# Kernel optimization log

Measured on AMD Instinct MI355X. Metric: run time of the kernel, lower is better.

The kernel has to match this reference:

```python
import jax, jax.numpy as jnp
import numpy as np

NUM_HEADS = 12
HIDDEN = 768
HEAD = HIDDEN // NUM_HEADS
SCALE = HIDDEN ** (-0.5)  # NB: module scales by hidden_dim**-0.5, not head_size**-0.5


def setup_inputs() -> dict:
    key = jax.random.key(0)
    ks = jax.random.split(key, 8)
    B, N = 16, 512
    std = HIDDEN ** (-0.5)
    return {
        "x": jax.random.normal(ks[0], (B, N, HIDDEN), dtype=jnp.float32),
        "encoding_bias": jax.random.normal(ks[1], (B, N, N), dtype=jnp.float32),
        "Wq": jax.random.normal(ks[2], (HIDDEN, HIDDEN), dtype=jnp.float32) * std,
        "Wk": jax.random.normal(ks[3], (HIDDEN, HIDDEN), dtype=jnp.float32) * std,
        "Wv": jax.random.normal(ks[4], (HIDDEN, HIDDEN), dtype=jnp.float32) * std,
        "bv": jax.random.normal(ks[5], (HIDDEN,), dtype=jnp.float32) * 0.01,
        "Wo": jax.random.normal(ks[6], (HIDDEN, HIDDEN), dtype=jnp.float32) * std,
        "bo": jax.random.normal(ks[7], (HIDDEN,), dtype=jnp.float32) * 0.01,
    }


def reference(x, encoding_bias, Wq, Wk, Wv, bv, Wo, bo):
    B, N, _ = x.shape
    # torch nn.Linear: y = x @ W.T (+ b)
    q = (x @ Wq.T).reshape(B, N, NUM_HEADS, HEAD)
    k = (x @ Wk.T).reshape(B, N, NUM_HEADS, HEAD)
    v = (x @ Wv.T + bv).reshape(B, N, NUM_HEADS, HEAD)
    # scores: [B, H, N, N] with additive graph bias broadcast over heads
    a = jnp.einsum("bnhd,bmhd->bhnm", q, k) * SCALE + encoding_bias[:, None, :, :]
    # data-dependent pad mask: rows whose scores are identically zero
    pad_mask = jnp.all(a == 0, axis=-1)  # [B, H, N]
    a = jnp.where(pad_mask[..., None], -jnp.inf, a)
    a = jax.nn.softmax(a, axis=-1)
    a = jnp.nan_to_num(a)  # all -inf rows -> NaN -> 0
    o = jnp.einsum("bhnm,bmhd->bnhd", a, v).reshape(B, N, HIDDEN)
    # dropout is identity in eval mode
    return o @ Wo.T + bo
```

## Files before the change

### kernel.cpp

```cpp
#include <hip/hip_runtime.h>
#include <stdint.h>

typedef unsigned short u16;
typedef unsigned int u32;
typedef __bf16 bf16x8 __attribute__((ext_vector_type(8)));
typedef float f32x4 __attribute__((ext_vector_type(4)));

#define NH 12
#define HD 64
#define SEQ 512
#define BATCH 16
#define HID 768
#define SCALE_Q 0.03608439182435161f

__device__ __forceinline__ u16 f2bf(float f) {
    u32 u = __builtin_bit_cast(u32, f);
    u32 r = (u + 0x7FFFu + ((u >> 16) & 1u)) >> 16;
    return (u16)r;
}
__device__ __forceinline__ float bf2f(u16 h) {
    return __builtin_bit_cast(float, (u32)h << 16);
}

__device__ __forceinline__ void gl2lds16(const u16* g, u16* lds_base) {
    __builtin_amdgcn_global_load_lds(
        (const __attribute__((address_space(1))) u32*)g,
        (__attribute__((address_space(3))) u32*)lds_base, 16, 0, 0);
}

#define NXB 6144
#define NEB 4096
#define NWB 576
__global__ void cvt_all(const float* __restrict__ x, const float* __restrict__ eb,
                        const float* __restrict__ w0, const float* __restrict__ w1,
                        const float* __restrict__ w2, const float* __restrict__ w3,
                        u16* __restrict__ dst) {
    int b = blockIdx.x;
    const float* s; int sb;
    if (b < NXB) { s = x; sb = 0; }
    else if (b < NXB + NEB) { s = eb; sb = NXB; }
    else if (b < NXB + NEB + NWB) { s = w0; sb = NXB + NEB; }
    else if (b < NXB + NEB + 2 * NWB) { s = w1; sb = NXB + NEB + NWB; }
    else if (b < NXB + NEB + 3 * NWB) { s = w2; sb = NXB + NEB + 2 * NWB; }
    else { s = w3; sb = NXB + NEB + 3 * NWB; }
    int li = (b - sb) * 1024 + threadIdx.x * 4;
    float4 v = *(const float4*)(s + li);
    ushort4 o;
    o.x = f2bf(v.x); o.y = f2bf(v.y); o.z = f2bf(v.z); o.w = f2bf(v.w);
    *(ushort4*)(dst + (size_t)b * 1024 + threadIdx.x * 4) = o;
}

__device__ __forceinline__ void stage_gemm(
    const u16* __restrict__ Ag, const u16* __restrict__ Bg, int k0,
    u16* As, u16* Bs, int r0, int q0, int r1, int q1, int w)
{
    gl2lds16(Ag + (size_t)r0 * HID + k0 + q0, As + w * 512);
    gl2lds16(Ag + (size_t)r1 * HID + k0 + q1, As + 2048 + w * 512);
    gl2lds16(Bg + (size_t)r0 * HID + k0 + q0, Bs + w * 512);
    gl2lds16(Bg + (size_t)r1 * HID + k0 + q1, Bs + 2048 + w * 512);
}

__device__ __forceinline__ void gemm_mainloop(
    const u16* __restrict__ Ag, const u16* __restrict__ Bg,
    u16 (*As)[128 * 32], u16 (*Bs)[128 * 32], f32x4 (&acc)[4][4])
{
    const int tid = threadIdx.x;
    const int l = tid & 63, w = tid >> 6;
    const int wm = w & 1, wn = w >> 1;
    const int lr = l & 15, lg = l >> 4;

    const int c0 = tid, c1 = tid + 256;
    const int r0 = c0 >> 2, q0 = (((c0 & 3) ^ ((r0 >> 1) & 3)) * 8);
    const int r1 = c1 >> 2, q1 = (((c1 & 3) ^ ((r1 >> 1) & 3)) * 8);

    const int sA = (lg ^ ((lr >> 1) & 3)) * 8;

    stage_gemm(Ag, Bg, 0, As[0], Bs[0], r0, q0, r1, q1, w);
    stage_gemm(Ag, Bg, 32, As[1], Bs[1], r0, q0, r1, q1, w);

    int cur = 0;
    for (int i = 0; i < 24; i++) {
        if (i < 23)
            asm volatile("s_waitcnt vmcnt(4) lgkmcnt(0)" ::: "memory");
        else
            asm volatile("s_waitcnt vmcnt(0) lgkmcnt(0)" ::: "memory");
        __builtin_amdgcn_s_barrier();
        __builtin_amdgcn_sched_barrier(0);

        int nxt = cur + 2; if (nxt >= 3) nxt -= 3;
        if (i < 22)
            stage_gemm(Ag, Bg, (i + 2) * 32, As[nxt], Bs[nxt], r0, q0, r1, q1, w);

        bf16x8 af[4], bfr[4];
#pragma unroll
        for (int mi = 0; mi < 4; mi++)
            af[mi] = *(const bf16x8*)(As[cur] + (wm * 64 + mi * 16 + lr) * 32 + sA);
#pragma unroll
        for (int ni = 0; ni < 4; ni++)
            bfr[ni] = *(const bf16x8*)(Bs[cur] + (wn * 64 + ni * 16 + lr) * 32 + sA);
#pragma unroll
        for (int mi = 0; mi < 4; mi++)
#pragma unroll
            for (int ni = 0; ni < 4; ni++)
                acc[mi][ni] = __builtin_amdgcn_mfma_f32_16x16x32_bf16(af[mi], bfr[ni], acc[mi][ni], 0, 0, 0);

        cur += 1; if (cur >= 3) cur -= 3;
    }
}

__global__ __launch_bounds__(256, 3) void gemm_qkv(
    const u16* __restrict__ xb, const u16* __restrict__ wq,
    const u16* __restrict__ wk, const u16* __restrict__ wv,
    const float* __restrict__ bv,
    u16* __restrict__ qtb, u16* __restrict__ kb, u16* __restrict__ vtb)
{
    __shared__ __align__(16) u16 As[3][128 * 32];
    __shared__ __align__(16) u16 Bs[3][128 * 32];
    const int tid = threadIdx.x;
    const int l = tid & 63, w = tid >> 6;
    const int wm = w & 1, wn = w >> 1;
    const int lr = l & 15, lg = l >> 4;
    const int mt = blockIdx.x, nt = blockIdx.y, z = blockIdx.z;

    const u16* Bw = (z == 0) ? wq : (z == 1) ? wk : wv;
    const u16* Ag = xb + (size_t)(mt * 128) * HID;
    const u16* Bg = Bw + (size_t)(nt * 128) * HID;

    f32x4 acc[4][4] = {};
    gemm_mainloop(Ag, Bg, As, Bs, acc);

    const float sc = (z == 0) ? SCALE_Q : 1.0f;
#pragma unroll
    for (int mi = 0; mi < 4; mi++) {
#pragma unroll
        for (int ni = 0; ni < 4; ni++) {
            const int jg = nt * 128 + wn * 64 + ni * 16 + lr;
            const int h = jg >> 6, d = jg & 63;
            const int i0 = mt * 128 + wm * 64 + mi * 16 + lg * 4;
            const int b = i0 >> 9, n0 = i0 & 511;
            if (z == 1) {
#pragma unroll
                for (int r2 = 0; r2 < 4; r2++)
                    kb[((size_t)(b * NH + h) * SEQ + n0 + r2) * HD + d] = f2bf(acc[mi][ni][r2]);
            } else {
                float bb = (z == 2) ? bv[jg] : 0.0f;
                ushort4 pk;
                pk.x = f2bf(fmaf(acc[mi][ni][0], sc, bb));
                pk.y = f2bf(fmaf(acc[mi][ni][1], sc, bb));
                pk.z = f2bf(fmaf(acc[mi][ni][2], sc, bb));
                pk.w = f2bf(fmaf(acc[mi][ni][3], sc, bb));
                u16* O = (z == 0) ? qtb : vtb;
                *(ushort4*)(O + ((size_t)(b * NH + h) * HD + d) * SEQ + n0) = pk;
            }
        }
    }
}

__global__ __launch_bounds__(256, 3) void gemm_out(
    const u16* __restrict__ A, const u16* __restrict__ wo,
    const float* __restrict__ bo, float* __restrict__ Cout)
{
    __shared__ __align__(16) u16 As[3][128 * 32];
    __shared__ __align__(16) u16 Bs[3][128 * 32];
    const int tid = threadIdx.x;
    const int l = tid & 63, w = tid >> 6;
    const int wm = w & 1, wn = w >> 1;
    const int lr = l & 15, lg = l >> 4;

    const int L = blockIdx.x;
    const int xcd = L & 7, s = L >> 3;
    const int nt = s >> 3;
    const int mt = xcd * 8 + (s & 7);

    const u16* Ag = A + (size_t)(mt * 128) * HID;
    const u16* Bg = wo + (size_t)(nt * 128) * HID;

    f32x4 acc[4][4] = {};
    gemm_mainloop(Ag, Bg, As, Bs, acc);

#pragma unroll
    for (int mi = 0; mi < 4; mi++) {
#pragma unroll
        for (int ni = 0; ni < 4; ni++) {
            const int jg = nt * 128 + wn * 64 + ni * 16 + lr;
            float bb = bo[jg];
#pragma unroll
            for (int r2 = 0; r2 < 4; r2++) {
                int ig = mt * 128 + wm * 64 + mi * 16 + lg * 4 + r2;
                Cout[(size_t)ig * HID + jg] = acc[mi][ni][r2] + bb;
            }
        }
    }
}

__device__ __forceinline__ void stage_kv(
    const u16* __restrict__ Kg, const u16* __restrict__ Vg, int mt0,
    u16* Ksb, u16* Vsb, int kr0, int kc0, int kr1, int kc1, int w)
{
    gl2lds16(Kg + (size_t)(mt0 + kr0) * HD + kc0 * 8, Ksb + w * 512);
    gl2lds16(Kg + (size_t)(mt0 + kr1) * HD + kc1 * 8, Ksb + 2048 + w * 512);
    gl2lds16(Vg + (size_t)kr0 * SEQ + mt0 + kc0 * 8, Vsb + w * 512);
    gl2lds16(Vg + (size_t)kr1 * SEQ + mt0 + kc1 * 8, Vsb + 2048 + w * 512);
}

__global__ __launch_bounds__(256, 3) void attn_kernel(
    const u16* __restrict__ qtb, const u16* __restrict__ kb, const u16* __restrict__ vtb,
    const u16* __restrict__ ebb, u16* __restrict__ ob)
{
    __shared__ __align__(16) u16 Ks[2][64 * 64];
    __shared__ __align__(16) u16 Vs[2][64 * 64];
    __shared__ __align__(16) u16 Ps[8][16 * 64];

    const int tid = threadIdx.x;
    const int l = tid & 63, w = tid >> 6;
    const int lr = l & 15, lg = l >> 4;

    const int L = blockIdx.x;
    const int xcd = L & 7, s = L >> 3;
    const int b = xcd * 2 + (s / 48);
    const int s2 = s % 48;
    const int h = s2 >> 2, qt = s2 & 3;

    const int bh = b * NH + h;
    const int qrow0 = qt * 128 + w * 16;

    const u16* Kg = kb + (size_t)bh * SEQ * HD;
    const u16* Vg = vtb + (size_t)bh * HD * SEQ;
    const u16* Eg0 = ebb + ((size_t)b * SEQ + qrow0 + lg * 4) * SEQ;
    const u16* Eg1 = Eg0 + (size_t)64 * SEQ;

    const int p0 = tid, p1 = tid + 256;
    const int kr0 = p0 >> 3, kc0 = (p0 & 7) ^ (kr0 & 7);
    const int kr1 = p1 >> 3, kc1 = (p1 & 7) ^ (kr1 & 7);

    stage_kv(Kg, Vg, 0, Ks[0], Vs[0], kr0, kc0, kr1, kc1, w);

    const u16* Qg = qtb + (size_t)bh * HD * SEQ + qrow0 + lr;
    bf16x8 qA0, qA1, qB0, qB1;
#pragma unroll
    for (int j = 0; j < 8; j++) {
        qA0[j] = __builtin_bit_cast(__bf16, Qg[(size_t)(lg * 8 + j) * SEQ]);
        qA1[j] = __builtin_bit_cast(__bf16, Qg[(size_t)(lg * 8 + j + 32) * SEQ]);
        qB0[j] = __builtin_bit_cast(__bf16, Qg[(size_t)(lg * 8 + j) * SEQ + 64]);
        qB1[j] = __builtin_bit_cast(__bf16, Qg[(size_t)(lg * 8 + j + 32) * SEQ + 64]);
    }

    bf16x8 ones;
#pragma unroll
    for (int j = 0; j < 8; j++) ones[j] = __builtin_bit_cast(__bf16, (u16)0x3F80);

    f32x4 oacc0[4] = {}, oacc1[4] = {};
    f32x4 lacc0 = {}, lacc1 = {};
    float amax0[4] = {0.f, 0.f, 0.f, 0.f};
    float amax1[4] = {0.f, 0.f, 0.f, 0.f};
    u16* Pw0 = Ps[w];
    u16* Pw1 = Ps[4 + w];

    for (int t = 0; t < 8; t++) {
        const int cur = t & 1;
        const int mt0 = t * 64;
        __syncthreads();

        u16 bl0[4][4], bl1[4][4];
#pragma unroll
        for (int mi = 0; mi < 4; mi++)
#pragma unroll
            for (int r = 0; r < 4; r++) {
                bl0[mi][r] = Eg0[(size_t)r * SEQ + mt0 + mi * 16 + lr];
                bl1[mi][r] = Eg1[(size_t)r * SEQ + mt0 + mi * 16 + lr];
            }

        if (t < 7)
            stage_kv(Kg, Vg, mt0 + 64, Ks[cur ^ 1], Vs[cur ^ 1], kr0, kc0, kr1, kc1, w);

        float sm0[4][4], sm1[4][4];
#pragma unroll
        for (int mi = 0; mi < 4; mi++) {
            const int row = mi * 16 + lr;
            bf16x8 kf0 = *(const bf16x8*)(Ks[cur] + row * 64 + ((lg ^ (row & 7)) * 8));
            bf16x8 kf1 = *(const bf16x8*)(Ks[cur] + row * 64 + (((4 + lg) ^ (row & 7)) * 8));
            f32x4 s0, s1;
#pragma unroll
            for (int r = 0; r < 4; r++) { s0[r] = bf2f(bl0[mi][r]); s1[r] = bf2f(bl1[mi][r]); }
            s0 = __builtin_amdgcn_mfma_f32_16x16x32_bf16(qA0, kf0, s0, 0, 0, 0);
            s0 = __builtin_amdgcn_mfma_f32_16x16x32_bf16(qA1, kf1, s0, 0, 0, 0);
            s1 = __builtin_amdgcn_mfma_f32_16x16x32_bf16(qB0, kf0, s1, 0, 0, 0);
            s1 = __builtin_amdgcn_mfma_f32_16x16x32_bf16(qB1, kf1, s1, 0, 0, 0);
#pragma unroll
            for (int r = 0; r < 4; r++) {
                float a = s0[r], c = s1[r];
                amax0[r] = fmaxf(amax0[r], fabsf(a));
                amax1[r] = fmaxf(amax1[r], fabsf(c));
                sm0[mi][r] = __expf(a);
                sm1[mi][r] = __expf(c);
            }
        }

#pragma unroll
        for (int mi = 0; mi < 4; mi++)
#pragma unroll
            for (int r = 0; r < 4; r++) {
                const int q = lg * 4 + r;
                const int chunk = mi * 2 + (lr >> 3);
                const int off = q * 64 + ((chunk ^ (q & 7)) * 8) + (lr & 7);
                Pw0[off] = f2bf(sm0[mi][r]);
                Pw1[off] = f2bf(sm1[mi][r]);
            }

#pragma unroll
        for (int ks = 0; ks < 2; ks++) {
            bf16x8 pf0 = *(const bf16x8*)(Pw0 + lr * 64 + (((ks * 4 + lg) ^ (lr & 7)) * 8));
            bf16x8 pf1 = *(const bf16x8*)(Pw1 + lr * 64 + (((ks * 4 + lg) ^ (lr & 7)) * 8));
#pragma unroll
            for (int di = 0; di < 4; di++) {
                const int row = di * 16 + lr;
                bf16x8 vf = *(const bf16x8*)(Vs[cur] + row * 64 + (((ks * 4 + lg) ^ (row & 7)) * 8));
                oacc0[di] = __builtin_amdgcn_mfma_f32_16x16x32_bf16(pf0, vf, oacc0[di], 0, 0, 0);
                oacc1[di] = __builtin_amdgcn_mfma_f32_16x16x32_bf16(pf1, vf, oacc1[di], 0, 0, 0);
            }
            lacc0 = __builtin_amdgcn_mfma_f32_16x16x32_bf16(pf0, ones, lacc0, 0, 0, 0);
            lacc1 = __builtin_amdgcn_mfma_f32_16x16x32_bf16(pf1, ones, lacc1, 0, 0, 0);
        }
    }

#pragma unroll
    for (int r = 0; r < 4; r++) {
        float am0 = amax0[r], am1 = amax1[r];
        am0 = fmaxf(am0, __shfl_xor(am0, 1));
        am0 = fmaxf(am0, __shfl_xor(am0, 2));
        am0 = fmaxf(am0, __shfl_xor(am0, 4));
        am0 = fmaxf(am0, __shfl_xor(am0, 8));
        am1 = fmaxf(am1, __shfl_xor(am1, 1));
        am1 = fmaxf(am1, __shfl_xor(am1, 2));
        am1 = fmaxf(am1, __shfl_xor(am1, 4));
        am1 = fmaxf(am1, __shfl_xor(am1, 8));
        float inv0 = (am0 > 0.f) ? (1.0f / lacc0[r]) : 0.0f;
        float inv1 = (am1 > 0.f) ? (1.0f / lacc1[r]) : 0.0f;
        int n0 = qrow0 + lg * 4 + r;
        u16* orow0 = ob + ((size_t)b * SEQ + n0) * HID + h * HD;
        u16* orow1 = ob + ((size_t)b * SEQ + n0 + 64) * HID + h * HD;
#pragma unroll
        for (int di = 0; di < 4; di++) {
            orow0[di * 16 + lr] = f2bf(oacc0[di][r] * inv0);
            orow1[di * 16 + lr] = f2bf(oacc1[di][r] * inv1);
        }
    }
}

extern "C" void kernel_launch(void* const* d_in, const int* in_sizes, int n_in,
                              void* d_out, int out_size, void* d_ws, size_t ws_size,
                              hipStream_t stream) {
    (void)in_sizes; (void)n_in; (void)out_size; (void)ws_size;
    const float* x  = (const float*)d_in[0];
    const float* eb = (const float*)d_in[1];
    const float* Wq = (const float*)d_in[2];
    const float* Wk = (const float*)d_in[3];
    const float* Wv = (const float*)d_in[4];
    const float* bv = (const float*)d_in[5];
    const float* Wo = (const float*)d_in[6];
    const float* bo = (const float*)d_in[7];
    float* out = (float*)d_out;

    const int NX = BATCH * SEQ * HID;
    const int NW = HID * HID;
    const int NE = BATCH * SEQ * SEQ;
    u16* ws   = (u16*)d_ws;
    u16* xb   = ws;
    u16* ebb  = xb + NX;
    u16* wqb  = ebb + NE;
    u16* wkb  = wqb + NW;
    u16* wvb  = wkb + NW;
    u16* wob  = wvb + NW;
    u16* qtb  = wob + NW;
    u16* kb   = qtb + NX;
    u16* vtb  = kb + NX;
    u16* obuf = vtb + NX;

    cvt_all<<<NXB + NEB + 4 * NWB, 256, 0, stream>>>(x, eb, Wq, Wk, Wv, Wo, ws);

    gemm_qkv<<<dim3(64, 6, 3), 256, 0, stream>>>(xb, wqb, wkb, wvb, bv, qtb, kb, vtb);

    attn_kernel<<<768, 256, 0, stream>>>(qtb, kb, vtb, ebb, obuf);

    gemm_out<<<384, 256, 0, stream>>>(obuf, wob, bo, out);
}
```

Measured before the change: 198.0 us.

## Fuse Q/K/V projection blocks so one 768-thread block shares the x tile

The QKV GEMM now runs as one 768-thread block per (m,n) tile instead of three separate 256-thread blocks. Each group of four waves computes one of Q, K or V, and all groups read a single shared LDS copy of the x tile. This cuts the global loads and LDS staging of the activation tile by a factor of three. In exchange, LDS per block grows to about 96KB, and launch_bounds(768,3) may not be achievable, so occupancy could drop and register pressure could rise.

```diff
diff --git a/kernel.cpp b/kernel.cpp
--- a/kernel.cpp
+++ b/kernel.cpp
@@ -50,6 +50,111 @@
     *(ushort4*)(dst + (size_t)b * 1024 + threadIdx.x * 4) = o;
 }
 
+__global__ __launch_bounds__(768, 3) void gemm_qkv(
+    const u16* __restrict__ xb, const u16* __restrict__ wq,
+    const u16* __restrict__ wk, const u16* __restrict__ wv,
+    const float* __restrict__ bv,
+    u16* __restrict__ qtb, u16* __restrict__ kb, u16* __restrict__ vtb)
+{
+    __shared__ __align__(16) u16 As[3][4096];
+    __shared__ __align__(16) u16 Bs[3][3][4096];
+    const int tid = threadIdx.x;
+    const int l = tid & 63, w = tid >> 6;
+    const int wz = w >> 2, wl = w & 3;
+    const int wm = wl & 1, wn = wl >> 1;
+    const int lr = l & 15, lg = l >> 4;
+    const int mt = blockIdx.x, nt = blockIdx.y;
+
+    const u16* Ag = xb + (size_t)(mt * 128) * HID;
+    const u16* Bg0 = wq + (size_t)(nt * 128) * HID;
+    const u16* Bg1 = wk + (size_t)(nt * 128) * HID;
+    const u16* Bg2 = wv + (size_t)(nt * 128) * HID;
+
+    const int sl0 = (w < 8) ? (w * 64 + l) : ((w - 8) * 64 + l);
+    const int r0 = sl0 >> 2, q0 = (((sl0 & 3) ^ ((r0 >> 1) & 3)) * 8);
+    const u16* s0 = ((w < 8) ? Ag : Bg0) + (size_t)r0 * HID + q0;
+    const int d0off = (w < 8) ? (w * 512) : ((w - 8) * 512);
+    const int sl1 = (w < 4) ? (256 + w * 64 + l) : ((w - 4) * 64 + l);
+    const int r1 = sl1 >> 2, q1 = (((sl1 & 3) ^ ((r1 >> 1) & 3)) * 8);
+    const u16* s1 = ((w < 4) ? Bg0 : Bg1) + (size_t)r1 * HID + q1;
+    const int d1off = (w < 4) ? (2048 + w * 512) : ((w - 4) * 512);
+    const int sl2 = w * 64 + l;
+    const int r2s = sl2 >> 2, q2 = (((sl2 & 3) ^ ((r2s >> 1) & 3)) * 8);
+    const u16* s2 = Bg2 + (size_t)r2s * HID + q2;
+    const int d2off = w * 512;
+
+    const int sA = (lg ^ ((lr >> 1) & 3)) * 8;
+
+#define STAGE_QKV(k0, buf)                                                      \
+    do {                                                                        \
+        gl2lds16(s0 + (k0), ((w < 8) ? As[buf] : Bs[0][buf]) + d0off);          \
+        gl2lds16(s1 + (k0), ((w < 4) ? Bs[0][buf] : Bs[1][buf]) + d1off);       \
+        if (w < 8) gl2lds16(s2 + (k0), Bs[2][buf] + d2off);                     \
+    } while (0)
+
+    STAGE_QKV(0, 0);
+    STAGE_QKV(32, 1);
+
+    f32x4 acc[4][4] = {};
+    int cur = 0;
+    for (int i = 0; i < 24; i++) {
+        if (i < 23) {
+            if (w < 8) asm volatile("s_waitcnt vmcnt(3) lgkmcnt(0)" ::: "memory");
+            else       asm volatile("s_waitcnt vmcnt(2) lgkmcnt(0)" ::: "memory");
+        } else {
+            asm volatile("s_waitcnt vmcnt(0) lgkmcnt(0)" ::: "memory");
+        }
+        __builtin_amdgcn_s_barrier();
+        __builtin_amdgcn_sched_barrier(0);
+
+        int nxt = cur + 2; if (nxt >= 3) nxt -= 3;
+        if (i < 22)
+            STAGE_QKV((i + 2) * 32, nxt);
+
+        bf16x8 af[4], bfr[4];
+#pragma unroll
+        for (int mi = 0; mi < 4; mi++)
+            af[mi] = *(const bf16x8*)(As[cur] + (wm * 64 + mi * 16 + lr) * 32 + sA);
+#pragma unroll
+        for (int ni = 0; ni < 4; ni++)
+            bfr[ni] = *(const bf16x8*)(Bs[wz][cur] + (wn * 64 + ni * 16 + lr) * 32 + sA);
+#pragma unroll
+        for (int mi = 0; mi < 4; mi++)
+#pragma unroll
+            for (int ni = 0; ni < 4; ni++)
+                acc[mi][ni] = __builtin_amdgcn_mfma_f32_16x16x32_bf16(af[mi], bfr[ni], acc[mi][ni], 0, 0, 0);
+
+        cur += 1; if (cur >= 3) cur -= 3;
+    }
+#undef STAGE_QKV
+
+    const float sc = (wz == 0) ? SCALE_Q : 1.0f;
+#pragma unroll
+    for (int mi = 0; mi < 4; mi++) {
+#pragma unroll
+        for (int ni = 0; ni < 4; ni++) {
+            const int jg = nt * 128 + wn * 64 + ni * 16 + lr;
+            const int h = jg >> 6, d = jg & 63;
+            const int i0 = mt * 128 + wm * 64 + mi * 16 + lg * 4;
+            const int b = i0 >> 9, n0 = i0 & 511;
+            if (wz == 1) {
+#pragma unroll
+                for (int r2 = 0; r2 < 4; r2++)
+                    kb[((size_t)(b * NH + h) * SEQ + n0 + r2) * HD + d] = f2bf(acc[mi][ni][r2]);
+            } else {
+                float bb = (wz == 2) ? bv[jg] : 0.0f;
+                ushort4 pk;
+                pk.x = f2bf(fmaf(acc[mi][ni][0], sc, bb));
+                pk.y = f2bf(fmaf(acc[mi][ni][1], sc, bb));
+                pk.z = f2bf(fmaf(acc[mi][ni][2], sc, bb));
+                pk.w = f2bf(fmaf(acc[mi][ni][3], sc, bb));
+                u16* O = (wz == 0) ? qtb : vtb;
+                *(ushort4*)(O + ((size_t)(b * NH + h) * HD + d) * SEQ + n0) = pk;
+            }
+        }
+    }
+}
+
 __device__ __forceinline__ void stage_gemm(
     const u16* __restrict__ Ag, const u16* __restrict__ Bg, int k0,
     u16* As, u16* Bs, int r0, int q0, int r1, int q1, int w)
@@ -105,54 +210,6 @@
                 acc[mi][ni] = __builtin_amdgcn_mfma_f32_16x16x32_bf16(af[mi], bfr[ni], acc[mi][ni], 0, 0, 0);
 
         cur += 1; if (cur >= 3) cur -= 3;
-    }
-}
-
-__global__ __launch_bounds__(256, 3) void gemm_qkv(
-    const u16* __restrict__ xb, const u16* __restrict__ wq,
-    const u16* __restrict__ wk, const u16* __restrict__ wv,
-    const float* __restrict__ bv,
-    u16* __restrict__ qtb, u16* __restrict__ kb, u16* __restrict__ vtb)
-{
-    __shared__ __align__(16) u16 As[3][128 * 32];
-    __shared__ __align__(16) u16 Bs[3][128 * 32];
-    const int tid = threadIdx.x;
-    const int l = tid & 63, w = tid >> 6;
-    const int wm = w & 1, wn = w >> 1;
-    const int lr = l & 15, lg = l >> 4;
-    const int mt = blockIdx.x, nt = blockIdx.y, z = blockIdx.z;
-
-    const u16* Bw = (z == 0) ? wq : (z == 1) ? wk : wv;
-    const u16* Ag = xb + (size_t)(mt * 128) * HID;
-    const u16* Bg = Bw + (size_t)(nt * 128) * HID;
-
-    f32x4 acc[4][4] = {};
-    gemm_mainloop(Ag, Bg, As, Bs, acc);
-
-    const float sc = (z == 0) ? SCALE_Q : 1.0f;
-#pragma unroll
-    for (int mi = 0; mi < 4; mi++) {
-#pragma unroll
-        for (int ni = 0; ni < 4; ni++) {
-            const int jg = nt * 128 + wn * 64 + ni * 16 + lr;
-            const int h = jg >> 6, d = jg & 63;
-            const int i0 = mt * 128 + wm * 64 + mi * 16 + lg * 4;
-            const int b = i0 >> 9, n0 = i0 & 511;
-            if (z == 1) {
-#pragma unroll
-                for (int r2 = 0; r2 < 4; r2++)
-                    kb[((size_t)(b * NH + h) * SEQ + n0 + r2) * HD + d] = f2bf(acc[mi][ni][r2]);
-            } else {
-                float bb = (z == 2) ? bv[jg] : 0.0f;
-                ushort4 pk;
-                pk.x = f2bf(fmaf(acc[mi][ni][0], sc, bb));
-                pk.y = f2bf(fmaf(acc[mi][ni][1], sc, bb));
-                pk.z = f2bf(fmaf(acc[mi][ni][2], sc, bb));
-                pk.w = f2bf(fmaf(acc[mi][ni][3], sc, bb));
-                u16* O = (z == 0) ? qtb : vtb;
-                *(ushort4*)(O + ((size_t)(b * NH + h) * HD + d) * SEQ + n0) = pk;
-            }
-        }
     }
 }
 
@@ -378,7 +435,7 @@
 
     cvt_all<<<NXB + NEB + 4 * NWB, 256, 0, stream>>>(x, eb, Wq, Wk, Wv, Wo, ws);
 
-    gemm_qkv<<<dim3(64, 6, 3), 256, 0, stream>>>(xb, wqb, wkb, wvb, bv, qtb, kb, vtb);
+    gemm_qkv<<<dim3(64, 6), 768, 0, stream>>>(xb, wqb, wkb, wvb, bv, qtb, kb, vtb);
 
     attn_kernel<<<768, 256, 0, stream>>>(qtb, kb, vtb, ebb, obuf);
 
```

After: 197.6 us. Within noise of the previous version (-0.2%).
